# Performance work log

Hardware: AMD Instinct MI355X
Metric: run time of the kernel (lower is better)

## Reference

```python
import jax, jax.numpy as jnp
import numpy as np

D = 768  # inputdim = k_size = v_size (forced equal by residual + LayerNorm)
B, T = 16, 2048


def setup_inputs() -> dict:
    key = jax.random.key(0)
    ks = jax.random.split(key, 9)
    s = 1.0 / np.sqrt(D)
    return {
        "x": jax.random.normal(ks[0], (B, T, D), dtype=jnp.float32),
        "Wk": jax.random.normal(ks[1], (D, D), dtype=jnp.float32) * s,
        "bk": jnp.zeros((D,), dtype=jnp.float32),
        "Wq": jax.random.normal(ks[2], (D, D), dtype=jnp.float32) * s,
        "bq": jnp.zeros((D,), dtype=jnp.float32),
        "Wv": jax.random.normal(ks[3], (D, D), dtype=jnp.float32) * s,
        "bv": jnp.zeros((D,), dtype=jnp.float32),
        "gamma": jnp.ones((D,), dtype=jnp.float32),
        "beta": jnp.zeros((D,), dtype=jnp.float32),
    }


def reference(x, Wk, bk, Wq, bq, Wv, bv, gamma, beta):
    sq_k = jnp.sqrt(jnp.asarray(D, dtype=x.dtype))
    keys = jnp.einsum("btd,kd->btk", x, Wk) + bk      # [B,T,K]
    queries = jnp.einsum("btd,kd->btk", x, Wq) + bq   # [B,T,K]
    values = jnp.einsum("btd,vd->btv", x, Wv) + bv    # [B,T,V]
    logits = jnp.einsum("bqk,btk->bqt", queries, keys)  # [B,Tq,Tk]
    # NB: original softmaxes over dim=1 (the QUERY axis), then scales AFTER softmax
    q_k = jax.nn.softmax(logits, axis=1) / sq_k
    applied = jnp.einsum("bqt,btv->bqv", q_k, values)  # [B,T,V]
    y = applied + x
    mu = jnp.mean(y, axis=-1, keepdims=True)
    var = jnp.mean(jnp.square(y - mu), axis=-1, keepdims=True)
    return (y - mu) * jax.lax.rsqrt(var + 1e-5) * gamma + beta
```

## Files before the change

### kernel.cpp

```cpp
#include <hip/hip_runtime.h>
#include <hip/hip_fp16.h>

#define DD 768
#define BB 16
#define TT 2048
#define BT (BB*TT)
#define NQS 8

using u16 = unsigned short;
using f16 = _Float16;
typedef __attribute__((ext_vector_type(8))) f16 half8;
typedef __attribute__((ext_vector_type(4))) f16 half4;
typedef __attribute__((ext_vector_type(4))) float f32x4;

#define GSWZ(r) ((((r) & 3)) ^ (((r) >> 2) & 3))

typedef const __attribute__((address_space(1))) unsigned int* gas1;
typedef __attribute__((address_space(3))) unsigned int* las3;
__device__ __forceinline__ void gload16(const void* g, void* l){
  __builtin_amdgcn_global_load_lds((gas1)g, (las3)l, 16, 0, 0);
}

__global__ __launch_bounds__(256)
void tofp16_kernel(const float* __restrict__ src, f16* __restrict__ dst, int n4){
  const int stride = gridDim.x * 256;
  for (int i = blockIdx.x*256 + threadIdx.x; i < n4; i += stride){
    float4 v = ((const float4*)src)[i];
    half4 h; h[0]=(f16)v.x; h[1]=(f16)v.y; h[2]=(f16)v.z; h[3]=(f16)v.w;
    ((half4*)dst)[i] = h;
  }
}

template<int OMODE>
__global__ __launch_bounds__(256, OMODE==2 ? 3 : 2)
void gemmk(const f16* __restrict__ A, int lda, long sA,
           const f16* __restrict__ B, int ldb, long sB,
           void* __restrict__ Out, int ldc, long sC,
           const float* __restrict__ aux, int Kdim,
           float* __restrict__ f0, float* __restrict__ f1,
           const f16* __restrict__ cs)
{
  constexpr int MR = (OMODE==2) ? 4 : 8;
  constexpr int BM = MR * 32;
  constexpr int AC = BM / 64;

  __shared__ f16 lA[3][BM*32];
  __shared__ f16 lB[3][128*32];
  __shared__ float smx[OMODE==1 ? 4 : 1][4][16], szx[OMODE==1 ? 4 : 1][4][16];
  __shared__ f16 lCC[OMODE==2 ? 2048 : 8];

  const int nx = gridDim.x, ny = gridDim.y, nwg = nx * ny, cpx = nwg >> 3;
  int h = blockIdx.x + nx * blockIdx.y;
  h = (h & 7) * cpx + (h >> 3);
  const int bx = h / ny, by = h % ny;

  const int b = blockIdx.z;
  const f16* A_ = A + (size_t)b * sA;
  const f16* B_ = B + (size_t)b * sB;
  const int m0 = bx * BM, n0 = by * 128;
  const int tid = threadIdx.x, lane = tid & 63, wave = tid >> 6;
  const int wm = wave >> 1, wn = wave & 1;

  size_t gaO[AC], gbO[2];
#pragma unroll
  for (int k = 0; k < AC; ++k){
    int c = k*256 + tid, r = c >> 2, s = (c & 3) ^ GSWZ(r);
    gaO[k] = (size_t)(m0 + r) * lda + s * 8;
  }
#pragma unroll
  for (int k = 0; k < 2; ++k){
    int c = k*256 + tid, r = c >> 2, s = (c & 3) ^ GSWZ(r);
    gbO[k] = (size_t)(n0 + r) * ldb + s * 8;
  }

  f32x4 acc[MR][4] = {};
  const int NT = Kdim >> 5;

  auto STAGE = [&](int u, int kt){
#pragma unroll
    for (int k = 0; k < AC; ++k) gload16(A_ + gaO[k] + kt, &lA[u][(k*256+tid)*8]);
#pragma unroll
    for (int k = 0; k < 2; ++k)  gload16(B_ + gbO[k] + kt, &lB[u][(k*256+tid)*8]);
  };

  if constexpr (OMODE == 2){
    const f16* cb = cs + ((size_t)b * NQS + (bx >> 1)) * TT;
    ((half8*)lCC)[tid] = ((const half8*)cb)[tid];
    __syncthreads();
  }

  STAGE(0, 0); STAGE(1, 32);

  const int frow = lane & 15;
  const int rsl = (((lane >> 4) ^ GSWZ(frow)) & 3) * 8;
  const int tsl = (lane >> 4) * 8;
  const int offA = (wm*(MR*16) + frow)*32 + rsl;
  const int offB = (wn*64 + frow)*32 + rsl;

  int u = 0;
  for (int t = 0; t < NT; ++t){
    int u2 = u + 2; if (u2 >= 3) u2 -= 3;
    __builtin_amdgcn_s_barrier();
    __builtin_amdgcn_sched_barrier(0);
    if (t + 2 < NT) STAGE(u2, (t + 2) * 32);
    const int rem = NT - 1 - t;
    if constexpr (AC == 4){
      if (rem >= 2)      asm volatile("s_waitcnt vmcnt(12)" ::: "memory");
      else if (rem == 1) asm volatile("s_waitcnt vmcnt(6)"  ::: "memory");
      else               asm volatile("s_waitcnt vmcnt(0)"  ::: "memory");
    } else {
      if (rem >= 2)      asm volatile("s_waitcnt vmcnt(8)" ::: "memory");
      else if (rem == 1) asm volatile("s_waitcnt vmcnt(4)" ::: "memory");
      else               asm volatile("s_waitcnt vmcnt(0)" ::: "memory");
    }
    __builtin_amdgcn_s_barrier();
    __builtin_amdgcn_sched_barrier(0);

    const f16* tA = &lA[u][0] + offA;
    const f16* tB = &lB[u][0] + offB;
    half8 af[MR], bf[4];
#pragma unroll
    for (int i = 0; i < MR; ++i) af[i] = *(const half8*)(tA + i*512);
#pragma unroll
    for (int j = 0; j < 4; ++j)  bf[j] = *(const half8*)(tB + j*512);
    if constexpr (OMODE == 2){
      half8 cc = *(const half8*)&lCC[t*32 + tsl];
#pragma unroll
      for (int i = 0; i < MR; ++i) af[i] *= cc;
    }
    __builtin_amdgcn_s_setprio(1);
#pragma unroll
    for (int i = 0; i < MR; ++i)
#pragma unroll
      for (int j = 0; j < 4; ++j)
        acc[i][j] = __builtin_amdgcn_mfma_f32_16x16x32_f16(af[i], bf[j], acc[i][j], 0,0,0);
    __builtin_amdgcn_s_setprio(0);
    u = (u + 1 == 3) ? 0 : u + 1;
  }

  const int kq4 = (lane >> 4) * 4;
  if constexpr (OMODE == 0 || OMODE == 2){
    f16* O = (f16*)Out + (size_t)b * sC;
#pragma unroll
    for (int j = 0; j < 4; ++j){
      const int gc = n0 + wn*64 + j*16 + frow;
      float bias_v = 0.f;
      if constexpr (OMODE == 0) bias_v = aux[b*DD + gc];
#pragma unroll
      for (int i = 0; i < MR; ++i)
#pragma unroll
        for (int r = 0; r < 4; ++r){
          const int gr = m0 + wm*(MR*16) + i*16 + kq4 + r;
          O[(size_t)gr*ldc + gc] = (f16)(acc[i][j][r] + bias_v);
        }
    }
  } else {
    f16* O = (f16*)Out + (size_t)b * sC;
    float Mb[4], Zb[4];
#pragma unroll
    for (int j = 0; j < 4; ++j){
      float mx = acc[0][j][0];
#pragma unroll
      for (int i = 0; i < MR; ++i)
#pragma unroll
        for (int r = 0; r < 4; ++r) mx = fmaxf(mx, acc[i][j][r]);
      mx = fmaxf(mx, __shfl_xor(mx, 16, 64));
      mx = fmaxf(mx, __shfl_xor(mx, 32, 64));
      if (lane < 16) smx[wave][j][lane] = mx;
      Mb[j] = mx;
    }
    __syncthreads();
#pragma unroll
    for (int j = 0; j < 4; ++j)
      Mb[j] = fmaxf(Mb[j], smx[wave ^ 2][j][frow]);
#pragma unroll
    for (int j = 0; j < 4; ++j){
      const int gc = n0 + wn*64 + j*16 + frow;
      float zz = 0.f;
#pragma unroll
      for (int i = 0; i < MR; ++i)
#pragma unroll
        for (int r = 0; r < 4; ++r){
          const int gr = m0 + wm*(MR*16) + i*16 + kq4 + r;
          float e = __expf(acc[i][j][r] - Mb[j]);
          zz += e;
          O[(size_t)gr*ldc + gc] = (f16)e;
        }
      zz += __shfl_xor(zz, 16, 64);
      zz += __shfl_xor(zz, 32, 64);
      if (lane < 16) szx[wave][j][lane] = zz;
      Zb[j] = zz;
    }
    __syncthreads();
    if (wm == 0 && lane < 16){
#pragma unroll
      for (int j = 0; j < 4; ++j){
        const int gc = n0 + wn*64 + j*16 + lane;
        size_t o = ((size_t)b * NQS + bx) * TT + gc;
        f0[o] = Mb[j];
        f1[o] = Zb[j] + szx[wave + 2][j][lane];
      }
    }
  }
}

__global__ __launch_bounds__(256)
void statsB_kernel(const float* __restrict__ pm, const float* __restrict__ pz,
                   f16* __restrict__ c){
  const int b = blockIdx.y;
  const int t = blockIdx.x * 256 + threadIdx.x;
  float am[NQS], az[NQS];
#pragma unroll
  for (int k = 0; k < NQS; ++k){
    size_t o = ((size_t)b * NQS + k) * TT + t;
    am[k] = pm[o]; az[k] = pz[o];
  }
  float M = am[0];
#pragma unroll
  for (int k = 1; k < NQS; ++k) M = fmaxf(M, am[k]);
  float Z = 0.f;
#pragma unroll
  for (int k = 0; k < NQS; ++k) Z += az[k] * __expf(am[k] - M);
  const float zi = 1.f / (Z * 27.712812921102035f);
#pragma unroll
  for (int k = 0; k < NQS; ++k)
    c[((size_t)b * NQS + k) * TT + t] = (f16)(__expf(am[k] - M) * zi);
}

__global__ __launch_bounds__(256)
void transp_kernel(const u16* __restrict__ V, u16* __restrict__ Vt){
  const int b = blockIdx.z;
  const int t0 = blockIdx.x * 64, v0 = blockIdx.y * 64;
  const u16* Vb = V + (size_t)b * TT * DD;
  u16* Vtb = Vt + (size_t)b * DD * TT;
  __shared__ u16 tile[64][66];
  const int tid = threadIdx.x;
#pragma unroll
  for (int i = 0; i < 4; ++i){
    int cI = i*256 + tid;
    int r = cI >> 4, c4 = (cI & 15) * 4;
    ushort4 u = *(const ushort4*)&Vb[(size_t)(t0 + r) * DD + v0 + c4];
    tile[r][c4+0] = u.x; tile[r][c4+1] = u.y; tile[r][c4+2] = u.z; tile[r][c4+3] = u.w;
  }
  __syncthreads();
#pragma unroll
  for (int i = 0; i < 4; ++i){
    int cI = i*256 + tid;
    int vr = cI >> 4, t4 = (cI & 15) * 4;
    ushort4 u;
    u.x = tile[t4+0][vr]; u.y = tile[t4+1][vr]; u.z = tile[t4+2][vr]; u.w = tile[t4+3][vr];
    *(ushort4*)&Vtb[(size_t)(v0 + vr) * TT + t0 + t4] = u;
  }
}

__global__ __launch_bounds__(192)
void ln2_kernel(const half4* __restrict__ applied, const float4* __restrict__ x,
                const float4* __restrict__ gamma4, const float4* __restrict__ beta4,
                float4* __restrict__ out){
  const size_t base = (size_t)blockIdx.x * (DD/4);
  const int cc = threadIdx.x;
  half4 a4 = applied[base + cc];
  float4 x4 = x[base + cc];
  float y0 = (float)a4[0] + x4.x;
  float y1 = (float)a4[1] + x4.y;
  float y2 = (float)a4[2] + x4.z;
  float y3 = (float)a4[3] + x4.w;
  float s = y0+y1+y2+y3;
  float sq = y0*y0+y1*y1+y2*y2+y3*y3;
#pragma unroll
  for (int off = 32; off > 0; off >>= 1){
    s  += __shfl_down(s,  off, 64);
    sq += __shfl_down(sq, off, 64);
  }
  __shared__ float rs_[3], rq_[3];
  const int lane = threadIdx.x & 63, w = threadIdx.x >> 6;
  if (lane == 0){ rs_[w] = s; rq_[w] = sq; }
  __syncthreads();
  const float S_ = rs_[0]+rs_[1]+rs_[2];
  const float Q_ = rq_[0]+rq_[1]+rq_[2];
  const float mu  = S_ * (1.f/DD);
  const float var = Q_ * (1.f/DD) - mu*mu;
  const float rstd = rsqrtf(var + 1e-5f);
  float4 g = gamma4[cc], be = beta4[cc], o;
  o.x = (y0 - mu)*rstd*g.x + be.x;
  o.y = (y1 - mu)*rstd*g.y + be.y;
  o.z = (y2 - mu)*rstd*g.z + be.z;
  o.w = (y3 - mu)*rstd*g.w + be.w;
  out[base + cc] = o;
}

extern "C" void kernel_launch(void* const* d_in, const int* in_sizes, int n_in,
                              void* d_out, int out_size, void* d_ws, size_t ws_size,
                              hipStream_t stream)
{
  const float* x    = (const float*)d_in[0];
  const float* Wk   = (const float*)d_in[1];
  const float* bk   = (const float*)d_in[2];
  const float* Wq   = (const float*)d_in[3];
  const float* bq   = (const float*)d_in[4];
  const float* Wv   = (const float*)d_in[5];
  const float* bv   = (const float*)d_in[6];
  const float* gamma= (const float*)d_in[7];
  const float* beta = (const float*)d_in[8];
  float* out = (float*)d_out;

  const size_t PW = (size_t)DD*DD*2;
  const size_t PB = (size_t)TT*DD*2;
  const size_t T4 = (size_t)TT*4;
  auto al = [](size_t n){ return (n + 255) & ~(size_t)255; };

  auto need = [&](int G)->size_t{
    size_t t = al(3*PW) + al(3*DD*4) + al((size_t)BB*PB) + al((size_t)BB*TT*TT*2)
             + al((size_t)G*PB) + al(3*(size_t)G*PB)
             + 2*al((size_t)G*NQS*T4) + al((size_t)BB*NQS*TT*2);
    if (4*(size_t)G*PB < (size_t)BB*PB) t += al((size_t)BB*PB);
    return t;
  };

  int G = 0;
  for (int g : {16, 8, 4, 2, 1}) if (need(g) <= ws_size){ G = g; break; }
  if (G == 0) return;

  char* p = (char*)d_ws;
  auto alloc = [&](size_t n)->char*{ char* r = p; p += (n + 255) & ~(size_t)255; return r; };
  f16*   Wf    = (f16*)alloc(3*PW);
  float* biasf = (float*)alloc(3*DD*4);
  f16*   Vt    = (f16*)alloc((size_t)BB*PB);
  f16*   P16   = (f16*)alloc((size_t)BB*TT*TT*2);
  f16*   Xc    = (f16*)alloc((size_t)G*PB);
  f16*   QKVc  = (f16*)alloc(3*(size_t)G*PB);
  float* pm    = (float*)alloc((size_t)G*NQS*T4);
  float* pz    = (float*)alloc((size_t)G*NQS*T4);
  f16*   cbuf  = (f16*)alloc((size_t)BB*NQS*TT*2);
  f16* applied = (4*(size_t)G*PB >= (size_t)BB*PB) ? Xc
               : (f16*)alloc((size_t)BB*PB);
  f16* Qc = QKVc, *Kc = QKVc + (size_t)G*TT*DD, *Vc = QKVc + 2*(size_t)G*TT*DD;

  tofp16_kernel<<<288, 256, 0, stream>>>(Wq, Wf,             DD*DD/4);
  tofp16_kernel<<<288, 256, 0, stream>>>(Wk, Wf +   DD*DD,   DD*DD/4);
  tofp16_kernel<<<288, 256, 0, stream>>>(Wv, Wf + 2*DD*DD,   DD*DD/4);
  hipMemcpyAsync(biasf,        bq, DD*4, hipMemcpyDeviceToDevice, stream);
  hipMemcpyAsync(biasf +   DD, bk, DD*4, hipMemcpyDeviceToDevice, stream);
  hipMemcpyAsync(biasf + 2*DD, bv, DD*4, hipMemcpyDeviceToDevice, stream);

  const int nRows = G * TT;
  for (int b0 = 0; b0 < BB; b0 += G){
    tofp16_kernel<<<2048, 256, 0, stream>>>(x + (size_t)b0*TT*DD, Xc, nRows*DD/4);

    dim3 gp(nRows/256, DD/128, 3);
    gemmk<0><<<gp, 256, 0, stream>>>(Xc, DD, 0, Wf, DD, (long)DD*DD,
                                     QKVc, DD, (long)G*TT*DD, biasf, DD,
                                     nullptr, nullptr, nullptr);

    transp_kernel<<<dim3(TT/64, DD/64, G), 256, 0, stream>>>(
        (const u16*)Vc, (u16*)(Vt + (size_t)b0*DD*TT));

    dim3 gs(TT/256, TT/128, G);
    gemmk<1><<<gs, 256, 0, stream>>>(Qc, DD, (long)TT*DD, Kc, DD, (long)TT*DD,
                                     P16 + (size_t)b0*TT*TT, TT, (long)TT*TT,
                                     nullptr, DD, pm, pz, nullptr);

    statsB_kernel<<<dim3(TT/256, G), 256, 0, stream>>>(
        pm, pz, cbuf + (size_t)b0*NQS*TT);
  }

  dim3 gpv(TT/128, DD/128, BB);
  gemmk<2><<<gpv, 256, 0, stream>>>(P16, TT, (long)TT*TT, Vt, TT, (long)DD*TT,
                                    applied, DD, (long)TT*DD, nullptr, TT,
                                    nullptr, nullptr, cbuf);

  ln2_kernel<<<BT, 192, 0, stream>>>((const half4*)applied, (const float4*)x,
                                     (const float4*)gamma, (const float4*)beta,
                                     (float4*)out);
}
```

Baseline: 562.8 us.

## Stage GEMM epilogue through LDS for vector stores and fuse V transpose

```diff
diff --git a/kernel.cpp b/kernel.cpp
--- a/kernel.cpp
+++ b/kernel.cpp
@@ -6,8 +6,8 @@
 #define TT 2048
 #define BT (BB*TT)
 #define NQS 8
-
-using u16 = unsigned short;
+#define BST 76
+
 using f16 = _Float16;
 typedef __attribute__((ext_vector_type(8))) f16 half8;
 typedef __attribute__((ext_vector_type(4))) f16 half4;
@@ -38,7 +38,7 @@
            void* __restrict__ Out, int ldc, long sC,
            const float* __restrict__ aux, int Kdim,
            float* __restrict__ f0, float* __restrict__ f1,
-           const f16* __restrict__ cs)
+           const f16* __restrict__ cs, f16* __restrict__ vt)
 {
   constexpr int MR = (OMODE==2) ? 4 : 8;
   constexpr int BM = MR * 32;
@@ -138,25 +138,50 @@
     u = (u + 1 == 3) ? 0 : u + 1;
   }
 
+  __syncthreads();
   const int kq4 = (lane >> 4) * 4;
+  f16* bnc = &lA[0][0] + wave * (16*BST);
+  const int rrow = lane >> 2, rcol = (lane & 3) * 16;
+
   if constexpr (OMODE == 0 || OMODE == 2){
-    f16* O = (f16*)Out + (size_t)b * sC;
-#pragma unroll
-    for (int j = 0; j < 4; ++j){
-      const int gc = n0 + wn*64 + j*16 + frow;
-      float bias_v = 0.f;
-      if constexpr (OMODE == 0) bias_v = aux[b*DD + gc];
-#pragma unroll
-      for (int i = 0; i < MR; ++i)
-#pragma unroll
-        for (int r = 0; r < 4; ++r){
-          const int gr = m0 + wm*(MR*16) + i*16 + kq4 + r;
-          O[(size_t)gr*ldc + gc] = (f16)(acc[i][j][r] + bias_v);
-        }
+    const bool toVt = (OMODE == 0) && (b == 2);
+    float bias4[4] = {};
+    if constexpr (OMODE == 0){
+#pragma unroll
+      for (int j = 0; j < 4; ++j) bias4[j] = aux[b*DD + n0 + wn*64 + j*16 + frow];
+    }
+    f16* O = (OMODE == 0) ? ((f16*)Out + (size_t)b * sC) : ((f16*)Out + (size_t)b * sC);
+#pragma unroll
+    for (int i = 0; i < MR; ++i){
+#pragma unroll
+      for (int j = 0; j < 4; ++j)
+#pragma unroll
+        for (int r = 0; r < 4; ++r)
+          bnc[(kq4 + r)*BST + j*16 + frow] = (f16)(acc[i][j][r] + bias4[j]);
+      if (!toVt){
+        half8 w0 = *(const half8*)&bnc[rrow*BST + rcol];
+        half8 w1 = *(const half8*)&bnc[rrow*BST + rcol + 8];
+        const int gr = m0 + wm*(MR*16) + i*16 + rrow;
+        const int gc = n0 + wn*64 + rcol;
+        *(half8*)&O[(size_t)gr*ldc + gc]     = w0;
+        *(half8*)&O[(size_t)gr*ldc + gc + 8] = w1;
+      } else {
+        f16 tmp[16];
+#pragma unroll
+        for (int k = 0; k < 16; ++k) tmp[k] = bnc[k*BST + lane];
+        half8 v0, v1;
+#pragma unroll
+        for (int k = 0; k < 8; ++k){ v0[k] = tmp[k]; v1[k] = tmp[8+k]; }
+        const int tokg = m0 + wm*(MR*16) + i*16;
+        const int batch = tokg >> 11, tok = tokg & (TT-1);
+        f16* Vo = vt + ((size_t)batch*DD + n0 + wn*64 + lane)*TT + tok;
+        *(half8*)&Vo[0] = v0;
+        *(half8*)&Vo[8] = v1;
+      }
     }
   } else {
     f16* O = (f16*)Out + (size_t)b * sC;
-    float Mb[4], Zb[4];
+    float Mb[4];
 #pragma unroll
     for (int j = 0; j < 4; ++j){
       float mx = acc[0][j][0];
@@ -173,23 +198,29 @@
 #pragma unroll
     for (int j = 0; j < 4; ++j)
       Mb[j] = fmaxf(Mb[j], smx[wave ^ 2][j][frow]);
+    float zz[4] = {};
+#pragma unroll
+    for (int i = 0; i < MR; ++i){
+#pragma unroll
+      for (int j = 0; j < 4; ++j)
+#pragma unroll
+        for (int r = 0; r < 4; ++r){
+          float e = __expf(acc[i][j][r] - Mb[j]);
+          zz[j] += e;
+          bnc[(kq4 + r)*BST + j*16 + frow] = (f16)e;
+        }
+      half8 w0 = *(const half8*)&bnc[rrow*BST + rcol];
+      half8 w1 = *(const half8*)&bnc[rrow*BST + rcol + 8];
+      const int gr = m0 + wm*(MR*16) + i*16 + rrow;
+      const int gc = n0 + wn*64 + rcol;
+      *(half8*)&O[(size_t)gr*ldc + gc]     = w0;
+      *(half8*)&O[(size_t)gr*ldc + gc + 8] = w1;
+    }
 #pragma unroll
     for (int j = 0; j < 4; ++j){
-      const int gc = n0 + wn*64 + j*16 + frow;
-      float zz = 0.f;
-#pragma unroll
-      for (int i = 0; i < MR; ++i)
-#pragma unroll
-        for (int r = 0; r < 4; ++r){
-          const int gr = m0 + wm*(MR*16) + i*16 + kq4 + r;
-          float e = __expf(acc[i][j][r] - Mb[j]);
-          zz += e;
-          O[(size_t)gr*ldc + gc] = (f16)e;
-        }
-      zz += __shfl_xor(zz, 16, 64);
-      zz += __shfl_xor(zz, 32, 64);
-      if (lane < 16) szx[wave][j][lane] = zz;
-      Zb[j] = zz;
+      zz[j] += __shfl_xor(zz[j], 16, 64);
+      zz[j] += __shfl_xor(zz[j], 32, 64);
+      if (lane < 16) szx[wave][j][lane] = zz[j];
     }
     __syncthreads();
     if (wm == 0 && lane < 16){
@@ -198,7 +229,7 @@
         const int gc = n0 + wn*64 + j*16 + lane;
         size_t o = ((size_t)b * NQS + bx) * TT + gc;
         f0[o] = Mb[j];
-        f1[o] = Zb[j] + szx[wave + 2][j][lane];
+        f1[o] = zz[j] + szx[wave + 2][j][lane];
       }
     }
   }
@@ -225,32 +256,6 @@
 #pragma unroll
   for (int k = 0; k < NQS; ++k)
     c[((size_t)b * NQS + k) * TT + t] = (f16)(__expf(am[k] - M) * zi);
-}
-
-__global__ __launch_bounds__(256)
-void transp_kernel(const u16* __restrict__ V, u16* __restrict__ Vt){
-  const int b = blockIdx.z;
-  const int t0 = blockIdx.x * 64, v0 = blockIdx.y * 64;
-  const u16* Vb = V + (size_t)b * TT * DD;
-  u16* Vtb = Vt + (size_t)b * DD * TT;
-  __shared__ u16 tile[64][66];
-  const int tid = threadIdx.x;
-#pragma unroll
-  for (int i = 0; i < 4; ++i){
-    int cI = i*256 + tid;
-    int r = cI >> 4, c4 = (cI & 15) * 4;
-    ushort4 u = *(const ushort4*)&Vb[(size_t)(t0 + r) * DD + v0 + c4];
-    tile[r][c4+0] = u.x; tile[r][c4+1] = u.y; tile[r][c4+2] = u.z; tile[r][c4+3] = u.w;
-  }
-  __syncthreads();
-#pragma unroll
-  for (int i = 0; i < 4; ++i){
-    int cI = i*256 + tid;
-    int vr = cI >> 4, t4 = (cI & 15) * 4;
-    ushort4 u;
-    u.x = tile[t4+0][vr]; u.y = tile[t4+1][vr]; u.z = tile[t4+2][vr]; u.w = tile[t4+3][vr];
-    *(ushort4*)&Vtb[(size_t)(v0 + vr) * TT + t0 + t4] = u;
-  }
 }
 
 __global__ __launch_bounds__(192)
@@ -311,9 +316,9 @@
 
   auto need = [&](int G)->size_t{
     size_t t = al(3*PW) + al(3*DD*4) + al((size_t)BB*PB) + al((size_t)BB*TT*TT*2)
-             + al((size_t)G*PB) + al(3*(size_t)G*PB)
+             + al((size_t)G*PB) + al(2*(size_t)G*PB)
              + 2*al((size_t)G*NQS*T4) + al((size_t)BB*NQS*TT*2);
-    if (4*(size_t)G*PB < (size_t)BB*PB) t += al((size_t)BB*PB);
+    if (3*(size_t)G*PB < (size_t)BB*PB) t += al((size_t)BB*PB);
     return t;
   };
 
@@ -328,13 +333,13 @@
   f16*   Vt    = (f16*)alloc((size_t)BB*PB);
   f16*   P16   = (f16*)alloc((size_t)BB*TT*TT*2);
   f16*   Xc    = (f16*)alloc((size_t)G*PB);
-  f16*   QKVc  = (f16*)alloc(3*(size_t)G*PB);
+  f16*   QKVc  = (f16*)alloc(2*(size_t)G*PB);
   float* pm    = (float*)alloc((size_t)G*NQS*T4);
   float* pz    = (float*)alloc((size_t)G*NQS*T4);
   f16*   cbuf  = (f16*)alloc((size_t)BB*NQS*TT*2);
-  f16* applied = (4*(size_t)G*PB >= (size_t)BB*PB) ? Xc
+  f16* applied = (3*(size_t)G*PB >= (size_t)BB*PB) ? Xc
                : (f16*)alloc((size_t)BB*PB);
-  f16* Qc = QKVc, *Kc = QKVc + (size_t)G*TT*DD, *Vc = QKVc + 2*(size_t)G*TT*DD;
+  f16* Qc = QKVc, *Kc = QKVc + (size_t)G*TT*DD;
 
   tofp16_kernel<<<288, 256, 0, stream>>>(Wq, Wf,             DD*DD/4);
   tofp16_kernel<<<288, 256, 0, stream>>>(Wk, Wf +   DD*DD,   DD*DD/4);
@@ -350,15 +355,13 @@
     dim3 gp(nRows/256, DD/128, 3);
     gemmk<0><<<gp, 256, 0, stream>>>(Xc, DD, 0, Wf, DD, (long)DD*DD,
                                      QKVc, DD, (long)G*TT*DD, biasf, DD,
-                                     nullptr, nullptr, nullptr);
-
-    transp_kernel<<<dim3(TT/64, DD/64, G), 256, 0, stream>>>(
-        (const u16*)Vc, (u16*)(Vt + (size_t)b0*DD*TT));
+                                     nullptr, nullptr, nullptr,
+                                     Vt + (size_t)b0*DD*TT);
 
     dim3 gs(TT/256, TT/128, G);
     gemmk<1><<<gs, 256, 0, stream>>>(Qc, DD, (long)TT*DD, Kc, DD, (long)TT*DD,
                                      P16 + (size_t)b0*TT*TT, TT, (long)TT*TT,
-                                     nullptr, DD, pm, pz, nullptr);
+                                     nullptr, DD, pm, pz, nullptr, nullptr);
 
     statsB_kernel<<<dim3(TT/256, G), 256, 0, stream>>>(
         pm, pz, cbuf + (size_t)b0*NQS*TT);
@@ -367,7 +370,7 @@
   dim3 gpv(TT/128, DD/128, BB);
   gemmk<2><<<gpv, 256, 0, stream>>>(P16, TT, (long)TT*TT, Vt, TT, (long)DD*TT,
                                     applied, DD, (long)TT*DD, nullptr, TT,
-                                    nullptr, nullptr, cbuf);
+                                    nullptr, nullptr, cbuf, nullptr);
 
   ln2_kernel<<<BT, 192, 0, stream>>>((const half4*)applied, (const float4*)x,
                                      (const float4*)gamma, (const float4*)beta,
```

After: 538.8 us. 4.3% less time.
